# Optimization experiments

Measured on AMD Instinct MI355X. Metric: run time of the kernel, lower is better.

## Reference

```python
import jax, jax.numpy as jnp
import numpy as np

B, SEQ, D_MODEL, N_HEADS = 4, 4096, 1024, 16
HEAD_DIM = D_MODEL // N_HEADS


def setup_inputs() -> dict:
    key = jax.random.key(0)
    ks = jax.random.split(key, 12)
    d = D_MODEL
    s = 1.0 / np.sqrt(d)  # ~nn.Linear init scale
    f = lambda k, shape, sc=1.0: jax.random.normal(k, shape, dtype=jnp.float32) * sc
    return {
        "queries": f(ks[0], (B, SEQ, d)),
        "keys":    f(ks[1], (B, SEQ, d)),
        "values":  f(ks[2], (B, SEQ, d)),
        "Wr": f(ks[3], (d, d), s), "br": jnp.zeros((d,), jnp.float32),
        "Wk": f(ks[4], (d, d), s), "bk": jnp.zeros((d,), jnp.float32),
        "Wv": f(ks[5], (d, d), s), "bv": jnp.zeros((d,), jnp.float32),
        "Wo": f(ks[6], (d, d), s), "bo": jnp.zeros((d,), jnp.float32),
        "decay": f(ks[7], (N_HEADS, HEAD_DIM), 0.01) - 5.0,
        "bonus": jnp.zeros((N_HEADS, HEAD_DIM), jnp.float32),
    }


def reference(queries, keys, values, Wr, br, Wk, bk, Wv, bv, Wo, bo, decay, bonus):
    Bb, N, d = queries.shape
    M = keys.shape[1]
    H = decay.shape[0]
    Dh = d // H

    # projections (nn.Linear: x @ W^T + b), split into heads
    r = (queries @ Wr.T + br).reshape(Bb, N, H, Dh)              # (B,N,H,D)
    k = (keys    @ Wk.T + bk).reshape(Bb, M, H, Dh).transpose(1, 0, 2, 3)  # (M,B,H,D)
    v = (values  @ Wv.T + bv).reshape(Bb, M, H, Dh).transpose(1, 0, 2, 3)  # (M,B,H,D)

    decay_factor = jnp.exp(-jnp.exp(decay))  # exp(w), w = -exp(decay); (H,D)

    def step(carry, kv):
        num, den = carry                       # (B,H,D)
        k_t, v_t = kv                          # (B,H,D)
        kc = jnp.clip(k_t, -10.0, 10.0)
        ek = jnp.exp(kc)
        bonus_w = jnp.exp(bonus + kc)          # (B,H,D) via broadcast
        wkv_t = (num + bonus_w * v_t) / (den + bonus_w + 1e-6)
        num = num * decay_factor + ek * v_t
        den = den * decay_factor + ek
        return (num, den), wkv_t

    init = (jnp.zeros((Bb, H, Dh), queries.dtype), jnp.zeros((Bb, H, Dh), queries.dtype))
    _, wkv = jax.lax.scan(step, init, (k, v))   # (M,B,H,D); here M == N
    wkv = wkv[:N].transpose(1, 0, 2, 3)         # (B,N,H,D)

    out = (jax.nn.sigmoid(r) * wkv).reshape(Bb, N, d)
    return out @ Wo.T + bo
```

## Files before the change

### kernel.cpp

```cpp
#include <hip/hip_runtime.h>

#define T_SEQ   4096
#define DM      1024
#define NB      4
#define ROWS    (NB * T_SEQ)
#define NCH     64
#define LCH     (T_SEQ / NCH)

typedef unsigned short ushort_t;

typedef __attribute__((ext_vector_type(8))) short bf16x8;
typedef __attribute__((ext_vector_type(4))) float f32x4;

__device__ __forceinline__ float bf2f(ushort_t u) {
  return __uint_as_float(((unsigned int)u) << 16);
}
__device__ __forceinline__ ushort_t f2bf(float f) {
  unsigned int u = __float_as_uint(f);
  u += 0x7FFFu + ((u >> 16) & 1u);
  return (ushort_t)(u >> 16);
}
__device__ __forceinline__ unsigned cvtpk(float lo, float hi) {
  unsigned r;
  asm("v_cvt_pk_bf16_f32 %0, %1, %2" : "=v"(r) : "v"(lo), "v"(hi));
  return r;
}

__device__ __forceinline__ void async16(const void* g, void* l) {
  __builtin_amdgcn_global_load_lds(
      (const __attribute__((address_space(1))) unsigned int*)g,
      (__attribute__((address_space(3))) unsigned int*)l, 16, 0, 0);
}

__device__ __forceinline__ int fragoff(int row, int col) {
  int p = (((row >> 4) * 2 + (col >> 5)) << 10) + ((row & 15) << 6) + ((col & 31) << 1);
  return p ^ (((row >> 3) & 1) << 5);
}

__global__ __launch_bounds__(256)
void cvt_pack(const float* __restrict__ Wr, const float* __restrict__ Wk,
              const float* __restrict__ Wv, const float* __restrict__ Wo,
              const float* __restrict__ br, const float* __restrict__ bk,
              const float* __restrict__ bv, const float* __restrict__ bo,
              ushort_t* __restrict__ wb, float* __restrict__ biasP) {
  const int bid = blockIdx.x;
  if (bid < 2048) {
    const int n4 = (DM * DM);
    for (int i = bid * 256 + threadIdx.x; i < n4; i += 2048 * 256) {
      const int seg = i >> 18;
      const float* src = seg == 0 ? Wr : seg == 1 ? Wk : seg == 2 ? Wv : Wo;
      const float4 f = ((const float4*)src)[i & 262143];
      ushort4 o;
      o.x = f2bf(f.x); o.y = f2bf(f.y); o.z = f2bf(f.z); o.w = f2bf(f.w);
      ((ushort4*)wb)[i] = o;
    }
  } else {
    const int s = bid - 2048;
    const float* b = s == 0 ? br : s == 1 ? bk : s == 2 ? bv : bo;
    for (int i = threadIdx.x; i < DM; i += 256) biasP[s * DM + i] = b[i];
  }
}

template <typename OutT>
__global__ __launch_bounds__(512, 2)
void gemm256(const ushort_t* __restrict__ A, const ushort_t* __restrict__ W,
             const float* __restrict__ bias, OutT* __restrict__ C,
             const int M, const int N, const int K) {
  __shared__ char smem[131072];
  const int T = K >> 6;
  const int nwg = (M >> 8) * (N >> 8);
  const int wg  = ((int)blockIdx.x & 7) * (nwg >> 3) + ((int)blockIdx.x >> 3);
  const int ntn = N >> 8;
  const int tm = wg / ntn, tn = wg % ntn;
  const int m0 = tm << 8, n0 = tn << 8;
  const int tid  = threadIdx.x;
  const int lane = tid & 63;
  const int wave = tid >> 6;
  const int wm128 = (wave >> 2) * 128;
  const int wn64  = (wave & 3) * 64;
  const int r15 = lane & 15;
  const int kq8 = (lane >> 4) * 8;

  int srow[2], scol[2];
  #pragma unroll
  for (int rho = 0; rho < 2; ++rho) {
    int p  = rho * 8192 + tid * 16;
    int pp = p ^ (((p >> 9) & 1) << 5);
    int e  = pp >> 1;
    int S = e >> 9, inr = e & 511;
    srow[rho] = ((S >> 1) << 4) + (inr >> 5);
    scol[rho] = ((S & 1) << 5) + (inr & 31);
  }

  auto stageA = [&](int tile, int half) {
    const int boff = ((tile & 1) << 15) + (half << 14);
    #pragma unroll
    for (int rho = 0; rho < 2; ++rho) {
      const ushort_t* g = A + (size_t)(m0 + half * 128 + srow[rho]) * K + (tile << 6) + scol[rho];
      async16(g, &smem[boff + rho * 8192 + tid * 16]);
    }
  };
  auto stageB = [&](int tile, int half) {
    const int boff = 65536 + ((tile & 1) << 15) + (half << 14);
    #pragma unroll
    for (int rho = 0; rho < 2; ++rho) {
      const ushort_t* g = W + (size_t)(n0 + half * 128 + srow[rho]) * K + (tile << 6) + scol[rho];
      async16(g, &smem[boff + rho * 8192 + tid * 16]);
    }
  };

  f32x4 acc[8][4];
  #pragma unroll
  for (int i = 0; i < 8; ++i)
    #pragma unroll
    for (int j = 0; j < 4; ++j)
      acc[i][j] = (f32x4){0.f, 0.f, 0.f, 0.f};
  bf16x8 bf[4][2];

  stageA(0, 0); stageA(0, 1); stageB(0, 0); stageB(0, 1); stageB(1, 0); stageB(1, 1);
  asm volatile("s_waitcnt vmcnt(4)" ::: "memory");
  __builtin_amdgcn_s_barrier();

#define GPHASE(Q, STG, TAILW)                                                    \
  {                                                                              \
    bf16x8 af[2][2];                                                             \
    _Pragma("unroll") for (int fl = 0; fl < 2; ++fl)                             \
      _Pragma("unroll") for (int ks = 0; ks < 2; ++ks)                           \
        af[fl][ks] = *(const bf16x8*)&smem[abase +                               \
            fragoff(wm128 + ((2 * (Q) + fl) << 4) + r15, (ks << 5) + kq8)];      \
    if ((Q) == 0) {                                                              \
      _Pragma("unroll") for (int fj = 0; fj < 4; ++fj)                           \
        _Pragma("unroll") for (int ks = 0; ks < 2; ++ks)                         \
          bf[fj][ks] = *(const bf16x8*)&smem[bbase +                             \
              fragoff(wn64 + (fj << 4) + r15, (ks << 5) + kq8)];                 \
    }                                                                            \
    STG();                                                                       \
    __builtin_amdgcn_s_barrier();                                                \
    __builtin_amdgcn_s_setprio(1);                                               \
    _Pragma("unroll") for (int fl = 0; fl < 2; ++fl)                             \
      _Pragma("unroll") for (int fj = 0; fj < 4; ++fj)                           \
        _Pragma("unroll") for (int ks = 0; ks < 2; ++ks)                         \
          acc[2 * (Q) + fl][fj] = __builtin_amdgcn_mfma_f32_16x16x32_bf16(       \
              af[fl][ks], bf[fj][ks], acc[2 * (Q) + fl][fj], 0, 0, 0);           \
    __builtin_amdgcn_s_setprio(0);                                               \
    TAILW();                                                                     \
    __builtin_amdgcn_s_barrier();                                                \
  }

  for (int j = 0; j < T; ++j) {
    const int abase = (j & 1) << 15;
    const int bbase = 65536 + ((j & 1) << 15);
    const bool p1 = (j + 1 < T), p2 = (j + 2 < T);
    auto s0 = [&] { if (p1) stageA(j + 1, 0); };
    auto s1 = [&] { if (p1) stageA(j + 1, 1); };
    auto s2 = [&] { if (p2) stageB(j + 2, 0); };
    auto s3 = [&] { if (p2) stageB(j + 2, 1); };
    auto nw = [&] {};
    auto bwait = [&] {
      if (p2) asm volatile("s_waitcnt vmcnt(4)" ::: "memory");
      else    asm volatile("s_waitcnt vmcnt(0)" ::: "memory");
    };
    GPHASE(0, s0, nw);
    GPHASE(1, s1, nw);
    GPHASE(2, s2, nw);
    GPHASE(3, s3, bwait);
  }
#undef GPHASE

  float bias4[4];
  #pragma unroll
  for (int fj = 0; fj < 4; ++fj) bias4[fj] = bias[n0 + wn64 + fj * 16 + r15];
  #pragma unroll
  for (int fi = 0; fi < 8; ++fi) {
    const int row0 = m0 + wm128 + fi * 16 + (lane >> 4) * 4;
    #pragma unroll
    for (int fj = 0; fj < 4; ++fj) {
      const int col = n0 + wn64 + fj * 16 + r15;
      #pragma unroll
      for (int r = 0; r < 4; ++r) {
        const float v = acc[fi][fj][r] + bias4[fj];
        if constexpr (sizeof(OutT) == 2) C[(size_t)(row0 + r) * N + col] = f2bf(v);
        else                             C[(size_t)(row0 + r) * N + col] = v;
      }
    }
  }
}

__global__ __launch_bounds__(512, 2)
void gemm3p(const float* __restrict__ Aq, const float* __restrict__ Ak,
            const float* __restrict__ Av, const ushort_t* __restrict__ Wb,
            const float* __restrict__ biasP, ushort_t* __restrict__ Cb,
            const int M, const int N, const int K) {
  __shared__ char smem[163840];
  const int T = K >> 5;
  const int ntpg = (M >> 8) * (N >> 8);
  const int nwg  = 3 * ntpg;
  const int wg = ((int)blockIdx.x & 7) * (nwg >> 3) + ((int)blockIdx.x >> 3);
  const int g     = wg / ntpg;
  const int local = wg % ntpg;
  const int ntn = N >> 8;
  const int tm = local / ntn, tn = local % ntn;
  const int m0 = tm << 8, n0 = tn << 8;
  const float*    Af   = g == 0 ? Aq : (g == 1 ? Ak : Av);
  const ushort_t* W    = Wb + (size_t)g * N * K;
  const float*    bias = biasP + g * N;
  ushort_t*       C    = Cb + (size_t)g * M * N;

  const int tid  = threadIdx.x;
  const int lane = tid & 63;
  const int wave = tid >> 6;
  const int wm128 = (wave >> 2) * 128;
  const int wn64  = (wave & 3) * 64;
  const int r15 = lane & 15;
  const int kq8 = (lane >> 4) * 8;

  int arow[4], acol[4];
  #pragma unroll
  for (int rho = 0; rho < 4; ++rho) {
    const int p = (rho & 1) * 8192 + tid * 16;
    const int e = (p ^ (((p >> 9) & 1) << 5)) >> 1;
    const int S = e >> 9, inr = e & 511;
    const int srl = ((S >> 1) << 4) + (inr >> 5);
    const int E   = ((S & 1) << 5) + (inr & 31);
    arow[rho] = (rho >> 1) * 128 + srl;
    acol[rho] = ((E & 31) >> 3) * 8 + (E >> 5) * 4;
  }
  int brow[2], bcolE[2];
  #pragma unroll
  for (int rho = 0; rho < 2; ++rho) {
    const int p = rho * 8192 + tid * 16;
    const int e = (p ^ (((p >> 9) & 1) << 5)) >> 1;
    const int S = e >> 9, inr = e & 511;
    brow[rho]  = ((S >> 1) << 4) + (inr >> 5);
    bcolE[rho] = ((S & 1) << 5) + (inr & 31);
  }

  auto stageA = [&](int tile) {
    const int boff = (tile % 3) * 32768;
    #pragma unroll
    for (int rho = 0; rho < 4; ++rho) {
      const float* s = Af + (size_t)(m0 + arow[rho]) * K + (tile << 5) + acol[rho];
      async16(s, &smem[boff + (rho >> 1) * 16384 + (rho & 1) * 8192 + tid * 16]);
    }
  };
  auto stageBh = [&](int bt, int half) {
    const int boff = 98304 + (bt & 1) * 32768 + half * 16384;
    #pragma unroll
    for (int rho = 0; rho < 2; ++rho) {
      const ushort_t* s = W + (size_t)(n0 + half * 128 + brow[rho]) * K + (bt << 6) + bcolE[rho];
      async16(s, &smem[boff + rho * 8192 + tid * 16]);
    }
  };

  auto rdA = [&](int abase, int row) -> bf16x8 {
    const f32x4 lo = *(const f32x4*)&smem[abase + fragoff(row, kq8)];
    const f32x4 hi = *(const f32x4*)&smem[abase + fragoff(row, kq8 + 32)];
    union { uint4 u4; bf16x8 b; } cv;
    cv.u4.x = cvtpk(lo[0], lo[1]); cv.u4.y = cvtpk(lo[2], lo[3]);
    cv.u4.z = cvtpk(hi[0], hi[1]); cv.u4.w = cvtpk(hi[2], hi[3]);
    return cv.b;
  };

  f32x4 acc[8][4];
  #pragma unroll
  for (int i = 0; i < 8; ++i)
    #pragma unroll
    for (int j = 0; j < 4; ++j)
      acc[i][j] = (f32x4){0.f, 0.f, 0.f, 0.f};
  bf16x8 bfr[4];

  stageA(0); stageBh(0, 0); stageBh(0, 1); stageA(1);
  asm volatile("s_waitcnt vmcnt(4)" ::: "memory");
  __builtin_amdgcn_s_barrier();

  for (int j = 0; j < T; ++j) {
    const int curA = (j % 3) * 32768;
    const int curB = 98304 + ((j >> 1) & 1) * 32768;
    const int ks   = (j & 1) << 5;
    const bool pre  = (j + 2 < T);
    const bool even = !(j & 1);
    {
      bf16x8 af[4];
      #pragma unroll
      for (int q = 0; q < 4; ++q) af[q] = rdA(curA, wm128 + q * 16 + r15);
      #pragma unroll
      for (int fj = 0; fj < 4; ++fj)
        bfr[fj] = *(const bf16x8*)&smem[curB + fragoff(wn64 + (fj << 4) + r15, ks + kq8)];
      if (pre) { stageA(j + 2); if (even) stageBh((j >> 1) + 1, 0); }
      __builtin_amdgcn_s_barrier();
      __builtin_amdgcn_s_setprio(1);
      #pragma unroll
      for (int q = 0; q < 4; ++q)
        #pragma unroll
        for (int fj = 0; fj < 4; ++fj)
          acc[q][fj] = __builtin_amdgcn_mfma_f32_16x16x32_bf16(af[q], bfr[fj], acc[q][fj], 0, 0, 0);
      __builtin_amdgcn_s_setprio(0);
      __builtin_amdgcn_s_barrier();
    }
    {
      bf16x8 af[4];
      #pragma unroll
      for (int q = 0; q < 4; ++q) af[q] = rdA(curA, wm128 + 64 + q * 16 + r15);
      if (pre && even) stageBh((j >> 1) + 1, 1);
      __builtin_amdgcn_s_barrier();
      __builtin_amdgcn_s_setprio(1);
      #pragma unroll
      for (int q = 0; q < 4; ++q)
        #pragma unroll
        for (int fj = 0; fj < 4; ++fj)
          acc[4 + q][fj] = __builtin_amdgcn_mfma_f32_16x16x32_bf16(af[q], bfr[fj], acc[4 + q][fj], 0, 0, 0);
      __builtin_amdgcn_s_setprio(0);
      if (pre) {
        if (even) asm volatile("s_waitcnt vmcnt(8)" ::: "memory");
        else      asm volatile("s_waitcnt vmcnt(4)" ::: "memory");
      } else if (j + 1 < T) {
        asm volatile("s_waitcnt vmcnt(0)" ::: "memory");
      }
      __builtin_amdgcn_s_barrier();
    }
  }

  float bias4[4];
  #pragma unroll
  for (int fj = 0; fj < 4; ++fj) bias4[fj] = bias[n0 + wn64 + fj * 16 + r15];
  #pragma unroll
  for (int fi = 0; fi < 8; ++fi) {
    const int row0 = m0 + wm128 + fi * 16 + (lane >> 4) * 4;
    #pragma unroll
    for (int fj = 0; fj < 4; ++fj) {
      const int col = n0 + wn64 + fj * 16 + r15;
      #pragma unroll
      for (int r = 0; r < 4; ++r)
        C[(size_t)(row0 + r) * N + col] = f2bf(acc[fi][fj][r] + bias4[fj]);
    }
  }
}

__global__ __launch_bounds__(256)
void wkv_pass1(const ushort_t* __restrict__ kp, const ushort_t* __restrict__ vp,
               const float* __restrict__ decay,
               float* __restrict__ s_num, float* __restrict__ s_den) {
  const int tid = threadIdx.x;
  const int grp = blockIdx.x & 3;
  const int c   = (blockIdx.x >> 2) & (NCH - 1);
  const int b   = (int)blockIdx.x >> 8;
  const int ch  = grp * 256 + tid;
  const float df = __expf(-__expf(decay[ch]));
  size_t idx = (size_t)b * T_SEQ * DM + (size_t)(c * LCH) * DM + ch;
  float num = 0.f, den = 0.f;
  for (int u = 0; u < LCH; ++u, idx += DM) {
    float kf = bf2f(kp[idx]);
    kf = fminf(fmaxf(kf, -10.f), 10.f);
    const float ek = __expf(kf);
    const float vv = bf2f(vp[idx]);
    num = fmaf(num, df, ek * vv);
    den = fmaf(den, df, ek);
  }
  const size_t si = ((size_t)b * NCH + c) * DM + ch;
  s_num[si] = num;
  s_den[si] = den;
}

__global__ __launch_bounds__(256)
void wkv_pass2(const float* __restrict__ decay,
               float* __restrict__ s_num, float* __restrict__ s_den) {
  const int tid = threadIdx.x;
  const int grp = blockIdx.x & 3;
  const int b   = (int)blockIdx.x >> 2;
  const int ch  = grp * 256 + tid;
  const float dfL = __expf(-__expf(decay[ch]) * (float)LCH);
  float an = 0.f, ad = 0.f;
  size_t si = (size_t)b * NCH * DM + ch;
  for (int c = 0; c < NCH; ++c, si += DM) {
    const float ln = s_num[si], ld = s_den[si];
    s_num[si] = an; s_den[si] = ad;
    an = fmaf(an, dfL, ln);
    ad = fmaf(ad, dfL, ld);
  }
}

__global__ __launch_bounds__(256)
void wkv_pass3(const ushort_t* __restrict__ kp, const ushort_t* __restrict__ vp,
               ushort_t* rg, const float* __restrict__ decay,
               const float* __restrict__ bonus,
               const float* __restrict__ s_num, const float* __restrict__ s_den) {
  const int tid = threadIdx.x;
  const int grp = blockIdx.x & 3;
  const int c   = (blockIdx.x >> 2) & (NCH - 1);
  const int b   = (int)blockIdx.x >> 8;
  const int ch  = grp * 256 + tid;
  const float df = __expf(-__expf(decay[ch]));
  const float eb = __expf(bonus[ch]);
  const size_t si = ((size_t)b * NCH + c) * DM + ch;
  float num = s_num[si], den = s_den[si];
  size_t idx = (size_t)b * T_SEQ * DM + (size_t)(c * LCH) * DM + ch;
  for (int u = 0; u < LCH; ++u, idx += DM) {
    float kf = bf2f(kp[idx]);
    kf = fminf(fmaxf(kf, -10.f), 10.f);
    const float ek = __expf(kf);
    const float bw = eb * ek;
    const float vv = bf2f(vp[idx]);
    const float rr = bf2f(rg[idx]);
    const float numer = fmaf(bw, vv, num);
    const float denom = den + bw + 1e-6f;
    const float wkv = numer * __builtin_amdgcn_rcpf(denom);
    const float sig = __builtin_amdgcn_rcpf(1.f + __expf(-rr));
    rg[idx] = f2bf(sig * wkv);
    num = fmaf(num, df, ek * vv);
    den = fmaf(den, df, ek);
  }
}

extern "C" void kernel_launch(void* const* d_in, const int* in_sizes, int n_in,
                              void* d_out, int out_size, void* d_ws, size_t ws_size,
                              hipStream_t stream) {
  const float* q   = (const float*)d_in[0];
  const float* ky  = (const float*)d_in[1];
  const float* vl  = (const float*)d_in[2];
  const float* Wr  = (const float*)d_in[3];
  const float* br  = (const float*)d_in[4];
  const float* Wk  = (const float*)d_in[5];
  const float* bk  = (const float*)d_in[6];
  const float* Wv  = (const float*)d_in[7];
  const float* bv  = (const float*)d_in[8];
  const float* Wo  = (const float*)d_in[9];
  const float* bo  = (const float*)d_in[10];
  const float* decay = (const float*)d_in[11];
  const float* bonus = (const float*)d_in[12];
  float* out = (float*)d_out;

  const size_t NE = (size_t)ROWS * DM;
  const size_t WE = (size_t)DM * DM;

  ushort_t* wb = (ushort_t*)d_ws;
  float* biasP = (float*)(wb + 4 * WE);
  ushort_t* rp = (ushort_t*)(biasP + 4 * DM);
  ushort_t* kp = rp + NE;
  ushort_t* vp = kp + NE;
  float* s_num = (float*)(vp + NE);
  float* s_den = s_num + (size_t)NB * NCH * DM;
  ushort_t* G  = rp;

  dim3 cB(256);
  dim3 gemmBlk(512);
  dim3 projGrid(3 * (ROWS / 256) * (DM / 256));
  dim3 gemmGrid((ROWS / 256) * (DM / 256));
  dim3 scanGrid(NB * NCH * (DM / 256)), scanBlk(256);

  cvt_pack<<<dim3(2052), cB, 0, stream>>>(Wr, Wk, Wv, Wo, br, bk, bv, bo, wb, biasP);
  gemm3p<<<projGrid, gemmBlk, 0, stream>>>(q, ky, vl, wb, biasP, rp, ROWS, DM, DM);
  wkv_pass1<<<scanGrid, scanBlk, 0, stream>>>(kp, vp, decay, s_num, s_den);
  wkv_pass2<<<dim3(NB * DM / 256), scanBlk, 0, stream>>>(decay, s_num, s_den);
  wkv_pass3<<<scanGrid, scanBlk, 0, stream>>>(kp, vp, rp, decay, bonus, s_num, s_den);
  gemm256<float><<<gemmGrid, gemmBlk, 0, stream>>>(G, wb + 3 * WE, biasP + 3 * DM, out, ROWS, DM, DM);
}
```

Before: 263.9 us.

## Replace 256x256 projection GEMM with 128x128-tile, double-buffered 256-thread kernel

The fused QKV projection GEMM moves from 256x256 tiles with 512 threads, a triple-buffered A and half-staged B pipeline, to 128x128 tiles with 256 threads. It uses simple double buffering of A (fp32) and B (bf16) per 32-wide K step, with one __syncthreads per iteration. The smaller tiles and 48KB of LDS allow several blocks per CU and a grid four times larger, aiming for better occupancy and load balance. In exchange each tile reuses its data less, so global/L2 traffic per FLOP goes up, and the shallower software pipeline may expose more load latency.

```diff
diff --git a/kernel.cpp b/kernel.cpp
--- a/kernel.cpp
+++ b/kernel.cpp
@@ -34,6 +34,10 @@
 
 __device__ __forceinline__ int fragoff(int row, int col) {
   int p = (((row >> 4) * 2 + (col >> 5)) << 10) + ((row & 15) << 6) + ((col & 31) << 1);
+  return p ^ (((row >> 3) & 1) << 5);
+}
+__device__ __forceinline__ int fragoffB32(int row, int col) {
+  int p = ((row >> 4) << 10) + ((row & 15) << 6) + (col << 1);
   return p ^ (((row >> 3) & 1) << 5);
 }
 
@@ -186,21 +190,21 @@
   }
 }
 
-__global__ __launch_bounds__(512, 2)
-void gemm3p(const float* __restrict__ Aq, const float* __restrict__ Ak,
-            const float* __restrict__ Av, const ushort_t* __restrict__ Wb,
-            const float* __restrict__ biasP, ushort_t* __restrict__ Cb,
-            const int M, const int N, const int K) {
-  __shared__ char smem[163840];
+__global__ __launch_bounds__(256, 3)
+void gemm128p(const float* __restrict__ Aq, const float* __restrict__ Ak,
+              const float* __restrict__ Av, const ushort_t* __restrict__ Wb,
+              const float* __restrict__ biasP, ushort_t* __restrict__ Cb,
+              const int M, const int N, const int K) {
+  __shared__ char smem[49152];
   const int T = K >> 5;
-  const int ntpg = (M >> 8) * (N >> 8);
+  const int ntpg = (M >> 7) * (N >> 7);
   const int nwg  = 3 * ntpg;
   const int wg = ((int)blockIdx.x & 7) * (nwg >> 3) + ((int)blockIdx.x >> 3);
   const int g     = wg / ntpg;
   const int local = wg % ntpg;
-  const int ntn = N >> 8;
+  const int ntn = N >> 7;
   const int tm = local / ntn, tn = local % ntn;
-  const int m0 = tm << 8, n0 = tn << 8;
+  const int m0 = tm << 7, n0 = tn << 7;
   const float*    Af   = g == 0 ? Aq : (g == 1 ? Ak : Av);
   const ushort_t* W    = Wb + (size_t)g * N * K;
   const float*    bias = biasP + g * N;
@@ -209,46 +213,42 @@
   const int tid  = threadIdx.x;
   const int lane = tid & 63;
   const int wave = tid >> 6;
-  const int wm128 = (wave >> 2) * 128;
-  const int wn64  = (wave & 3) * 64;
+  const int wr = (wave >> 1) * 64;
+  const int wc = (wave & 1) * 64;
   const int r15 = lane & 15;
   const int kq8 = (lane >> 4) * 8;
 
   int arow[4], acol[4];
   #pragma unroll
   for (int rho = 0; rho < 4; ++rho) {
-    const int p = (rho & 1) * 8192 + tid * 16;
+    const int p = rho * 4096 + tid * 16;
     const int e = (p ^ (((p >> 9) & 1) << 5)) >> 1;
     const int S = e >> 9, inr = e & 511;
-    const int srl = ((S >> 1) << 4) + (inr >> 5);
-    const int E   = ((S & 1) << 5) + (inr & 31);
-    arow[rho] = (rho >> 1) * 128 + srl;
-    acol[rho] = ((E & 31) >> 3) * 8 + (E >> 5) * 4;
-  }
-  int brow[2], bcolE[2];
+    arow[rho] = ((S >> 1) << 4) + (inr >> 5);
+    const int E = ((S & 1) << 5) + (inr & 31);
+    acol[rho] = (((E & 31) >> 3) << 3) + ((E >> 5) << 2);
+  }
+  int brow[2], bcol[2];
   #pragma unroll
   for (int rho = 0; rho < 2; ++rho) {
-    const int p = rho * 8192 + tid * 16;
-    const int e = (p ^ (((p >> 9) & 1) << 5)) >> 1;
-    const int S = e >> 9, inr = e & 511;
-    brow[rho]  = ((S >> 1) << 4) + (inr >> 5);
-    bcolE[rho] = ((S & 1) << 5) + (inr & 31);
-  }
-
-  auto stageA = [&](int tile) {
-    const int boff = (tile % 3) * 32768;
+    const int p = rho * 4096 + tid * 16;
+    const int pp = p ^ (((p >> 9) & 1) << 5);
+    brow[rho] = ((p >> 10) << 4) | ((pp >> 6) & 15);
+    bcol[rho] = (pp >> 1) & 31;
+  }
+
+  auto stage = [&](int tile) {
+    const int ab = (tile & 1) << 14;
     #pragma unroll
     for (int rho = 0; rho < 4; ++rho) {
       const float* s = Af + (size_t)(m0 + arow[rho]) * K + (tile << 5) + acol[rho];
-      async16(s, &smem[boff + (rho >> 1) * 16384 + (rho & 1) * 8192 + tid * 16]);
-    }
-  };
-  auto stageBh = [&](int bt, int half) {
-    const int boff = 98304 + (bt & 1) * 32768 + half * 16384;
+      async16(s, &smem[ab + rho * 4096 + tid * 16]);
+    }
+    const int bb = 32768 + ((tile & 1) << 13);
     #pragma unroll
     for (int rho = 0; rho < 2; ++rho) {
-      const ushort_t* s = W + (size_t)(n0 + half * 128 + brow[rho]) * K + (bt << 6) + bcolE[rho];
-      async16(s, &smem[boff + rho * 8192 + tid * 16]);
+      const ushort_t* s = W + (size_t)(n0 + brow[rho]) * K + (tile << 5) + bcol[rho];
+      async16(s, &smem[bb + rho * 4096 + tid * 16]);
     }
   };
 
@@ -261,74 +261,46 @@
     return cv.b;
   };
 
-  f32x4 acc[8][4];
-  #pragma unroll
-  for (int i = 0; i < 8; ++i)
+  f32x4 acc[4][4];
+  #pragma unroll
+  for (int i = 0; i < 4; ++i)
     #pragma unroll
     for (int j = 0; j < 4; ++j)
       acc[i][j] = (f32x4){0.f, 0.f, 0.f, 0.f};
-  bf16x8 bfr[4];
-
-  stageA(0); stageBh(0, 0); stageBh(0, 1); stageA(1);
-  asm volatile("s_waitcnt vmcnt(4)" ::: "memory");
-  __builtin_amdgcn_s_barrier();
-
-  for (int j = 0; j < T; ++j) {
-    const int curA = (j % 3) * 32768;
-    const int curB = 98304 + ((j >> 1) & 1) * 32768;
-    const int ks   = (j & 1) << 5;
-    const bool pre  = (j + 2 < T);
-    const bool even = !(j & 1);
-    {
-      bf16x8 af[4];
-      #pragma unroll
-      for (int q = 0; q < 4; ++q) af[q] = rdA(curA, wm128 + q * 16 + r15);
+
+  stage(0);
+  __syncthreads();
+
+  for (int t = 0; t < T; ++t) {
+    if (t + 1 < T) stage(t + 1);
+    const int ab = (t & 1) << 14;
+    const int bb = 32768 + ((t & 1) << 13);
+    bf16x8 af[4], bfr[4];
+    #pragma unroll
+    for (int q = 0; q < 4; ++q)
+      af[q] = rdA(ab, wr + q * 16 + r15);
+    #pragma unroll
+    for (int fj = 0; fj < 4; ++fj)
+      bfr[fj] = *(const bf16x8*)&smem[bb + fragoffB32(wc + (fj << 4) + r15, kq8)];
+    __builtin_amdgcn_s_setprio(1);
+    #pragma unroll
+    for (int q = 0; q < 4; ++q)
       #pragma unroll
       for (int fj = 0; fj < 4; ++fj)
-        bfr[fj] = *(const bf16x8*)&smem[curB + fragoff(wn64 + (fj << 4) + r15, ks + kq8)];
-      if (pre) { stageA(j + 2); if (even) stageBh((j >> 1) + 1, 0); }
-      __builtin_amdgcn_s_barrier();
-      __builtin_amdgcn_s_setprio(1);
-      #pragma unroll
-      for (int q = 0; q < 4; ++q)
-        #pragma unroll
-        for (int fj = 0; fj < 4; ++fj)
-          acc[q][fj] = __builtin_amdgcn_mfma_f32_16x16x32_bf16(af[q], bfr[fj], acc[q][fj], 0, 0, 0);
-      __builtin_amdgcn_s_setprio(0);
-      __builtin_amdgcn_s_barrier();
-    }
-    {
-      bf16x8 af[4];
-      #pragma unroll
-      for (int q = 0; q < 4; ++q) af[q] = rdA(curA, wm128 + 64 + q * 16 + r15);
-      if (pre && even) stageBh((j >> 1) + 1, 1);
-      __builtin_amdgcn_s_barrier();
-      __builtin_amdgcn_s_setprio(1);
-      #pragma unroll
-      for (int q = 0; q < 4; ++q)
-        #pragma unroll
-        for (int fj = 0; fj < 4; ++fj)
-          acc[4 + q][fj] = __builtin_amdgcn_mfma_f32_16x16x32_bf16(af[q], bfr[fj], acc[4 + q][fj], 0, 0, 0);
-      __builtin_amdgcn_s_setprio(0);
-      if (pre) {
-        if (even) asm volatile("s_waitcnt vmcnt(8)" ::: "memory");
-        else      asm volatile("s_waitcnt vmcnt(4)" ::: "memory");
-      } else if (j + 1 < T) {
-        asm volatile("s_waitcnt vmcnt(0)" ::: "memory");
-      }
-      __builtin_amdgcn_s_barrier();
-    }
+        acc[q][fj] = __builtin_amdgcn_mfma_f32_16x16x32_bf16(af[q], bfr[fj], acc[q][fj], 0, 0, 0);
+    __builtin_amdgcn_s_setprio(0);
+    __syncthreads();
   }
 
   float bias4[4];
   #pragma unroll
-  for (int fj = 0; fj < 4; ++fj) bias4[fj] = bias[n0 + wn64 + fj * 16 + r15];
-  #pragma unroll
-  for (int fi = 0; fi < 8; ++fi) {
-    const int row0 = m0 + wm128 + fi * 16 + (lane >> 4) * 4;
+  for (int fj = 0; fj < 4; ++fj) bias4[fj] = bias[n0 + wc + fj * 16 + r15];
+  #pragma unroll
+  for (int fi = 0; fi < 4; ++fi) {
+    const int row0 = m0 + wr + fi * 16 + (lane >> 4) * 4;
     #pragma unroll
     for (int fj = 0; fj < 4; ++fj) {
-      const int col = n0 + wn64 + fj * 16 + r15;
+      const int col = n0 + wc + fj * 16 + r15;
       #pragma unroll
       for (int r = 0; r < 4; ++r)
         C[(size_t)(row0 + r) * N + col] = f2bf(acc[fi][fj][r] + bias4[fj]);
@@ -442,13 +414,12 @@
   ushort_t* G  = rp;
 
   dim3 cB(256);
-  dim3 gemmBlk(512);
-  dim3 projGrid(3 * (ROWS / 256) * (DM / 256));
-  dim3 gemmGrid((ROWS / 256) * (DM / 256));
+  dim3 projGrid(3 * (ROWS / 128) * (DM / 128)), projBlk(256);
+  dim3 gemmGrid((ROWS / 256) * (DM / 256)), gemmBlk(512);
   dim3 scanGrid(NB * NCH * (DM / 256)), scanBlk(256);
 
   cvt_pack<<<dim3(2052), cB, 0, stream>>>(Wr, Wk, Wv, Wo, br, bk, bv, bo, wb, biasP);
-  gemm3p<<<projGrid, gemmBlk, 0, stream>>>(q, ky, vl, wb, biasP, rp, ROWS, DM, DM);
+  gemm128p<<<projGrid, projBlk, 0, stream>>>(q, ky, vl, wb, biasP, rp, ROWS, DM, DM);
   wkv_pass1<<<scanGrid, scanBlk, 0, stream>>>(kp, vp, decay, s_num, s_den);
   wkv_pass2<<<dim3(NB * DM / 256), scanBlk, 0, stream>>>(decay, s_num, s_den);
   wkv_pass3<<<scanGrid, scanBlk, 0, stream>>>(kp, vp, rp, decay, bonus, s_num, s_den);
```

Result: slower. 277.7 us (+5.2%).
